# Kernel tuning notes

Hardware: AMD Instinct MI355X
Metric: run time of the kernel (lower is better)

Reference implementation:

```python
import jax, jax.numpy as jnp
import numpy as np

N_QUBITS = 4
N_LAYERS = 6
BATCH = 1 << 20


def _apply_batched_1q(state, U, q):
    # state: [B, 2,2,2,2]; U: [B, 2, 2] per-sample gate on qubit q
    ax = q + 1
    s = jnp.moveaxis(state, ax, -1)
    s = jnp.einsum('bij,b...j->b...i', U, s)
    return jnp.moveaxis(s, -1, ax)


def _apply_shared_1q(state, U, q):
    # U: [2, 2] shared across the batch
    ax = q + 1
    s = jnp.moveaxis(state, ax, -1)
    s = jnp.einsum('ij,...j->...i', U, s)
    return jnp.moveaxis(s, -1, ax)


def _cnot(state, c, t):
    # flip target axis on the control=1 slice
    ca, ta = c + 1, t + 1
    s0 = jax.lax.index_in_dim(state, 0, ca, keepdims=True)
    s1 = jax.lax.index_in_dim(state, 1, ca, keepdims=True)
    return jnp.concatenate([s0, jnp.flip(s1, axis=ta)], axis=ca)


def _circuit(x, weights):
    n = N_QUBITS
    B = x.shape[0]
    # |0...0> state, batched: [B, 2,2,2,2]
    state = jnp.zeros((B,) + (2,) * n, dtype=jnp.complex64)
    state = state.at[(slice(None),) + (0,) * n].set(1.0)
    # Data-encoding RY(x_q) per sample on each wire
    half = x / 2
    c, s = jnp.cos(half), jnp.sin(half)  # [B, n]
    for q in range(n):
        row0 = jnp.stack([c[:, q], -s[:, q]], axis=-1)
        row1 = jnp.stack([s[:, q], c[:, q]], axis=-1)
        U = jnp.stack([row0, row1], axis=-2).astype(jnp.complex64)  # [B,2,2]
        state = _apply_batched_1q(state, U, q)
    # BasicEntanglerLayers: per layer, RX(w) on each wire then CNOT ring
    for l in range(weights.shape[0]):
        for q in range(n):
            t = weights[l, q] / 2
            ct = (jnp.cos(t) + 0j).astype(jnp.complex64)
            st = (-1j * jnp.sin(t)).astype(jnp.complex64)
            U = jnp.stack([jnp.stack([ct, st]), jnp.stack([st, ct])])  # [2,2]
            state = _apply_shared_1q(state, U, q)
        for q in range(n):
            state = _cnot(state, q, (q + 1) % n)
    # <Z_q> from marginal probabilities
    probs = jnp.real(state * jnp.conj(state))  # [B,2,2,2,2] float32
    z = jnp.array([1.0, -1.0], dtype=jnp.float32)
    outs = []
    for q in range(n):
        reduce_axes = tuple(a for a in range(1, n + 1) if a != q + 1)
        outs.append(jnp.tensordot(probs.sum(axis=reduce_axes), z, axes=([1], [0])))
    return jnp.stack(outs, axis=-1)  # [B, n_qubits]


def setup_inputs():
    key = jax.random.key(0)
    k1, k2 = jax.random.split(key)
    x = jax.random.normal(k1, (BATCH, N_QUBITS), dtype=jnp.float32)
    weights = jax.random.normal(k2, (N_LAYERS, N_QUBITS), dtype=jnp.float32) * 0.01
    return {"x": x, "weights": weights}


def reference(x, weights):
    return _circuit(x, weights)
```

## Files before the change

kernel.cpp:

```cpp
#include <hip/hip_runtime.h>
#include <math.h>

#define N_QUBITS 4
#define N_LAYERS 6
#define NW (N_LAYERS * N_QUBITS)
#define M 4

__global__ __launch_bounds__(256) void qprep_kernel(
    const float* __restrict__ weights, float* __restrict__ Ctab)
{
    __shared__ float Wr[16][16];
    __shared__ float Wi[16][16];
    __shared__ float S[4][16][16];
    __shared__ float wc[NW], ws[NW];
    const int tid = threadIdx.x;
    if (tid < NW) {
        float t = weights[tid] * 0.5f;
        wc[tid] = cosf(t);
        ws[tid] = sinf(t);
    }
    __syncthreads();

    if (tid < 16) {
        float re[16], im[16];
#pragma unroll
        for (int k = 0; k < 16; ++k) { re[k] = 0.f; im[k] = 0.f; }
        re[tid] = 1.f;
#pragma unroll
        for (int k = 0; k < 16; ++k) re[k] = (k == tid) ? 1.f : 0.f;
#pragma unroll
        for (int l = 0; l < N_LAYERS; ++l) {
#pragma unroll
            for (int q = 0; q < 4; ++q) {
                const float ct = wc[l * 4 + q], sn = ws[l * 4 + q];
                const int mask = 8 >> q;
#pragma unroll
                for (int idx = 0; idx < 16; ++idx) {
                    if (idx & mask) continue;
                    const int j = idx | mask;
                    float r0 = re[idx], u0 = im[idx], r1 = re[j], u1 = im[j];
                    re[idx] = ct * r0 + sn * u1; im[idx] = ct * u0 - sn * r1;
                    re[j]   = ct * r1 + sn * u0; im[j]   = ct * u1 - sn * r0;
                }
            }
#pragma unroll
            for (int q = 0; q < 4; ++q) {
                const int cm = 8 >> q, tm = 8 >> ((q + 1) & 3);
#pragma unroll
                for (int idx = 0; idx < 16; ++idx) {
                    if ((idx & cm) && !(idx & tm)) {
                        const int j = idx | tm;
                        float t0 = re[idx]; re[idx] = re[j]; re[j] = t0;
                        float t1 = im[idx]; im[idx] = im[j]; im[j] = t1;
                    }
                }
            }
        }
#pragma unroll
        for (int k = 0; k < 16; ++k) { Wr[k][tid] = re[k]; Wi[k][tid] = im[k]; }
    }
    __syncthreads();

    {
        const int i = tid >> 4, j = tid & 15;
        float acc0 = 0.f, acc1 = 0.f, acc2 = 0.f, acc3 = 0.f;
#pragma unroll
        for (int k = 0; k < 16; ++k) {
            const float prod = Wr[k][i] * Wr[k][j] + Wi[k][i] * Wi[k][j];
            acc0 += (k & 8) ? -prod : prod;
            acc1 += (k & 4) ? -prod : prod;
            acc2 += (k & 2) ? -prod : prod;
            acc3 += (k & 1) ? -prod : prod;
        }
        S[0][i][j] = acc0; S[1][i][j] = acc1; S[2][i][j] = acc2; S[3][i][j] = acc3;
    }
    __syncthreads();

    if (tid < 81) {
        const int t1 = tid / 27, t2 = (tid / 9) % 3, t3 = (tid / 3) % 3, t4 = tid % 3;
        int zm = 0, xm = 0;
        if (t1 == 1) zm |= 8; else if (t1 == 2) xm |= 8;
        if (t2 == 1) zm |= 4; else if (t2 == 2) xm |= 4;
        if (t3 == 1) zm |= 2; else if (t3 == 2) xm |= 2;
        if (t4 == 1) zm |= 1; else if (t4 == 2) xm |= 1;
#pragma unroll
        for (int q = 0; q < 4; ++q) {
            float acc = 0.f;
#pragma unroll
            for (int i = 0; i < 16; ++i) {
                const float v = S[q][i][i ^ xm];
                acc += (__popc(i & zm) & 1) ? -v : v;
            }
            Ctab[q * 81 + tid] = acc * 0.0625f;
        }
    }
}

__global__ __launch_bounds__(256) void qeval_kernel(
    const float* __restrict__ x, const float* __restrict__ Ctab,
    float* __restrict__ out, int B)
{
    const int tid = threadIdx.x;
    const int base = blockIdx.x * (256 * M) + tid;

    float4 xv[M];
#pragma unroll
    for (int m = 0; m < M; ++m) {
        const int b = base + m * 256;
        xv[m] = (b < B) ? reinterpret_cast<const float4*>(x)[b]
                        : make_float4(0.f, 0.f, 0.f, 0.f);
    }

    float vc[M][4], vs[M][4];
#pragma unroll
    for (int m = 0; m < M; ++m) {
        vc[m][0] = __cosf(xv[m].x); vs[m][0] = __sinf(xv[m].x);
        vc[m][1] = __cosf(xv[m].y); vs[m][1] = __sinf(xv[m].y);
        vc[m][2] = __cosf(xv[m].z); vs[m][2] = __sinf(xv[m].z);
        vc[m][3] = __cosf(xv[m].w); vs[m][3] = __sinf(xv[m].w);
    }

    float o[M][4];
#pragma unroll
    for (int q = 0; q < 4; ++q) {
        const float* __restrict__ Cq = Ctab + q * 81;
        float s1[M];
#pragma unroll
        for (int m = 0; m < M; ++m) s1[m] = 0.f;
#pragma unroll
        for (int t1 = 0; t1 < 3; ++t1) {
            float s2[M];
#pragma unroll
            for (int m = 0; m < M; ++m) s2[m] = 0.f;
#pragma unroll
            for (int t2 = 0; t2 < 3; ++t2) {
                float s3[M];
#pragma unroll
                for (int m = 0; m < M; ++m) s3[m] = 0.f;
#pragma unroll
                for (int t3 = 0; t3 < 3; ++t3) {
                    const int b3 = ((t1 * 3 + t2) * 3 + t3) * 3;
                    const float c0 = Cq[b3];
                    const float c1 = Cq[b3 + 1];
                    const float c2 = Cq[b3 + 2];
#pragma unroll
                    for (int m = 0; m < M; ++m) {
                        float e = c0;
                        e = fmaf(c1, vc[m][3], e);
                        e = fmaf(c2, vs[m][3], e);
                        if (t3 == 0)      s3[m] += e;
                        else if (t3 == 1) s3[m] = fmaf(e, vc[m][2], s3[m]);
                        else              s3[m] = fmaf(e, vs[m][2], s3[m]);
                    }
                }
#pragma unroll
                for (int m = 0; m < M; ++m) {
                    if (t2 == 0)      s2[m] += s3[m];
                    else if (t2 == 1) s2[m] = fmaf(s3[m], vc[m][1], s2[m]);
                    else              s2[m] = fmaf(s3[m], vs[m][1], s2[m]);
                }
            }
#pragma unroll
            for (int m = 0; m < M; ++m) {
                if (t1 == 0)      s1[m] += s2[m];
                else if (t1 == 1) s1[m] = fmaf(s2[m], vc[m][0], s1[m]);
                else              s1[m] = fmaf(s2[m], vs[m][0], s1[m]);
            }
        }
#pragma unroll
        for (int m = 0; m < M; ++m) o[m][q] = s1[m];
    }

#pragma unroll
    for (int m = 0; m < M; ++m) {
        const int b = base + m * 256;
        if (b < B)
            reinterpret_cast<float4*>(out)[b] =
                make_float4(o[m][0], o[m][1], o[m][2], o[m][3]);
    }
}

extern "C" void kernel_launch(void* const* d_in, const int* in_sizes, int n_in,
                              void* d_out, int out_size, void* d_ws, size_t ws_size,
                              hipStream_t stream) {
    const float* x = (const float*)d_in[0];
    const float* weights = (const float*)d_in[1];
    float* out = (float*)d_out;
    float* Ctab = (float*)d_ws;
    const int B = in_sizes[0] / 4;

    qprep_kernel<<<1, 256, 0, stream>>>(weights, Ctab);

    const int spb = 256 * M;
    const int grid = (B + spb - 1) / spb;
    qeval_kernel<<<grid, 256, 0, stream>>>(x, Ctab, out, B);
}
```

Before: 99.80 us.

## Interleave coefficient table per qubit and stage it in shared memory as float4

The coefficient table is rewritten so the four qubits' coefficients for each term sit next to each other as a float4. The eval kernel copies this table into LDS once per block and evaluates all four qubits in one pass over the 81-term tensor-product expansion. Previously each qubit had its own loop doing scalar uniform loads from global memory. The change replaces those scalar loads with vector LDS reads and shares the loop structure across qubits, at the cost of a block barrier, more live registers (float4 accumulators at three levels times M), and possibly lower occupancy.

```diff
diff --git a/kernel.cpp b/kernel.cpp
--- a/kernel.cpp
+++ b/kernel.cpp
@@ -24,10 +24,7 @@
     if (tid < 16) {
         float re[16], im[16];
 #pragma unroll
-        for (int k = 0; k < 16; ++k) { re[k] = 0.f; im[k] = 0.f; }
-        re[tid] = 1.f;
-#pragma unroll
-        for (int k = 0; k < 16; ++k) re[k] = (k == tid) ? 1.f : 0.f;
+        for (int k = 0; k < 16; ++k) { re[k] = (k == tid) ? 1.f : 0.f; im[k] = 0.f; }
 #pragma unroll
         for (int l = 0; l < N_LAYERS; ++l) {
 #pragma unroll
@@ -91,7 +88,7 @@
                 const float v = S[q][i][i ^ xm];
                 acc += (__popc(i & zm) & 1) ? -v : v;
             }
-            Ctab[q * 81 + tid] = acc * 0.0625f;
+            Ctab[tid * 4 + q] = acc * 0.0625f;
         }
     }
 }
@@ -100,83 +97,91 @@
     const float* __restrict__ x, const float* __restrict__ Ctab,
     float* __restrict__ out, int B)
 {
+    __shared__ float4 Cs[81];
     const int tid = threadIdx.x;
+    if (tid < 81) Cs[tid] = reinterpret_cast<const float4*>(Ctab)[tid];
+    __syncthreads();
+
     const int base = blockIdx.x * (256 * M) + tid;
 
-    float4 xv[M];
+    float vc[M][4], vs[M][4];
 #pragma unroll
     for (int m = 0; m < M; ++m) {
         const int b = base + m * 256;
-        xv[m] = (b < B) ? reinterpret_cast<const float4*>(x)[b]
-                        : make_float4(0.f, 0.f, 0.f, 0.f);
-    }
-
-    float vc[M][4], vs[M][4];
-#pragma unroll
-    for (int m = 0; m < M; ++m) {
-        vc[m][0] = __cosf(xv[m].x); vs[m][0] = __sinf(xv[m].x);
-        vc[m][1] = __cosf(xv[m].y); vs[m][1] = __sinf(xv[m].y);
-        vc[m][2] = __cosf(xv[m].z); vs[m][2] = __sinf(xv[m].z);
-        vc[m][3] = __cosf(xv[m].w); vs[m][3] = __sinf(xv[m].w);
-    }
-
-    float o[M][4];
-#pragma unroll
-    for (int q = 0; q < 4; ++q) {
-        const float* __restrict__ Cq = Ctab + q * 81;
-        float s1[M];
-#pragma unroll
-        for (int m = 0; m < M; ++m) s1[m] = 0.f;
-#pragma unroll
-        for (int t1 = 0; t1 < 3; ++t1) {
-            float s2[M];
-#pragma unroll
-            for (int m = 0; m < M; ++m) s2[m] = 0.f;
-#pragma unroll
-            for (int t2 = 0; t2 < 3; ++t2) {
-                float s3[M];
-#pragma unroll
-                for (int m = 0; m < M; ++m) s3[m] = 0.f;
-#pragma unroll
-                for (int t3 = 0; t3 < 3; ++t3) {
-                    const int b3 = ((t1 * 3 + t2) * 3 + t3) * 3;
-                    const float c0 = Cq[b3];
-                    const float c1 = Cq[b3 + 1];
-                    const float c2 = Cq[b3 + 2];
-#pragma unroll
-                    for (int m = 0; m < M; ++m) {
-                        float e = c0;
-                        e = fmaf(c1, vc[m][3], e);
-                        e = fmaf(c2, vs[m][3], e);
-                        if (t3 == 0)      s3[m] += e;
-                        else if (t3 == 1) s3[m] = fmaf(e, vc[m][2], s3[m]);
-                        else              s3[m] = fmaf(e, vs[m][2], s3[m]);
+        float4 xv = (b < B) ? reinterpret_cast<const float4*>(x)[b]
+                            : make_float4(0.f, 0.f, 0.f, 0.f);
+        vc[m][0] = __cosf(xv.x); vs[m][0] = __sinf(xv.x);
+        vc[m][1] = __cosf(xv.y); vs[m][1] = __sinf(xv.y);
+        vc[m][2] = __cosf(xv.z); vs[m][2] = __sinf(xv.z);
+        vc[m][3] = __cosf(xv.w); vs[m][3] = __sinf(xv.w);
+    }
+
+    float4 s1[M];
+#pragma unroll
+    for (int m = 0; m < M; ++m) s1[m] = make_float4(0.f, 0.f, 0.f, 0.f);
+
+#pragma unroll
+    for (int t1 = 0; t1 < 3; ++t1) {
+        float4 s2[M];
+#pragma unroll
+        for (int m = 0; m < M; ++m) s2[m] = make_float4(0.f, 0.f, 0.f, 0.f);
+#pragma unroll
+        for (int t2 = 0; t2 < 3; ++t2) {
+            float4 s3[M];
+#pragma unroll
+            for (int m = 0; m < M; ++m) s3[m] = make_float4(0.f, 0.f, 0.f, 0.f);
+#pragma unroll
+            for (int t3 = 0; t3 < 3; ++t3) {
+                const int b3 = ((t1 * 3 + t2) * 3 + t3) * 3;
+                const float4 c0 = Cs[b3];
+                const float4 c1 = Cs[b3 + 1];
+                const float4 c2 = Cs[b3 + 2];
+#pragma unroll
+                for (int m = 0; m < M; ++m) {
+                    const float a = vc[m][3], s = vs[m][3];
+                    float4 e;
+                    e.x = fmaf(c1.x, a, c0.x); e.y = fmaf(c1.y, a, c0.y);
+                    e.z = fmaf(c1.z, a, c0.z); e.w = fmaf(c1.w, a, c0.w);
+                    e.x = fmaf(c2.x, s, e.x);  e.y = fmaf(c2.y, s, e.y);
+                    e.z = fmaf(c2.z, s, e.z);  e.w = fmaf(c2.w, s, e.w);
+                    if (t3 == 0) {
+                        s3[m].x += e.x; s3[m].y += e.y; s3[m].z += e.z; s3[m].w += e.w;
+                    } else {
+                        const float w = (t3 == 1) ? vc[m][2] : vs[m][2];
+                        s3[m].x = fmaf(e.x, w, s3[m].x); s3[m].y = fmaf(e.y, w, s3[m].y);
+                        s3[m].z = fmaf(e.z, w, s3[m].z); s3[m].w = fmaf(e.w, w, s3[m].w);
                     }
                 }
-#pragma unroll
-                for (int m = 0; m < M; ++m) {
-                    if (t2 == 0)      s2[m] += s3[m];
-                    else if (t2 == 1) s2[m] = fmaf(s3[m], vc[m][1], s2[m]);
-                    else              s2[m] = fmaf(s3[m], vs[m][1], s2[m]);
-                }
             }
 #pragma unroll
             for (int m = 0; m < M; ++m) {
-                if (t1 == 0)      s1[m] += s2[m];
-                else if (t1 == 1) s1[m] = fmaf(s2[m], vc[m][0], s1[m]);
-                else              s1[m] = fmaf(s2[m], vs[m][0], s1[m]);
-            }
-        }
-#pragma unroll
-        for (int m = 0; m < M; ++m) o[m][q] = s1[m];
+                if (t2 == 0) {
+                    s2[m].x += s3[m].x; s2[m].y += s3[m].y;
+                    s2[m].z += s3[m].z; s2[m].w += s3[m].w;
+                } else {
+                    const float w = (t2 == 1) ? vc[m][1] : vs[m][1];
+                    s2[m].x = fmaf(s3[m].x, w, s2[m].x); s2[m].y = fmaf(s3[m].y, w, s2[m].y);
+                    s2[m].z = fmaf(s3[m].z, w, s2[m].z); s2[m].w = fmaf(s3[m].w, w, s2[m].w);
+                }
+            }
+        }
+#pragma unroll
+        for (int m = 0; m < M; ++m) {
+            if (t1 == 0) {
+                s1[m].x += s2[m].x; s1[m].y += s2[m].y;
+                s1[m].z += s2[m].z; s1[m].w += s2[m].w;
+            } else {
+                const float w = (t1 == 1) ? vc[m][0] : vs[m][0];
+                s1[m].x = fmaf(s2[m].x, w, s1[m].x); s1[m].y = fmaf(s2[m].y, w, s1[m].y);
+                s1[m].z = fmaf(s2[m].z, w, s1[m].z); s1[m].w = fmaf(s2[m].w, w, s1[m].w);
+            }
+        }
     }
 
 #pragma unroll
     for (int m = 0; m < M; ++m) {
         const int b = base + m * 256;
-        if (b < B)
-            reinterpret_cast<float4*>(out)[b] =
-                make_float4(o[m][0], o[m][1], o[m][2], o[m][3]);
+        if (b < B) reinterpret_cast<float4*>(out)[b] = s1[m];
     }
 }
 
```

New measurement: 126.4 us. 1.27x slower.
